# Optimization experiments

Measured on AMD Instinct MI355X. Metric: run time of the kernel, lower is better.

## Reference

```python
import jax, jax.numpy as jnp
import numpy as np

B = 4096       # batch
S = 4096       # seq_len == input_dim
DEPTH = 2
D_MODEL = 1
D_FFN = 2      # d_model * d_ffn_factor
EPS = 1e-5


def _layernorm(x, w, b):
    mu = jnp.mean(x, axis=-1, keepdims=True)
    var = jnp.mean((x - mu) ** 2, axis=-1, keepdims=True)
    return (x - mu) * jax.lax.rsqrt(var + EPS) * w + b


def setup_inputs() -> dict:
    key = jax.random.key(0)
    ks = jax.random.split(key, 16)
    sc = lambda fan_in: 1.0 / np.sqrt(fan_in)
    inp = {
        "x": jax.random.normal(ks[0], (B, S), dtype=jnp.float32),
        # per-depth stacked gMLP block params
        "ln1_w": jnp.ones((DEPTH, D_MODEL), jnp.float32),
        "ln1_b": jnp.zeros((DEPTH, D_MODEL), jnp.float32),
        "cp1_w": jax.random.uniform(ks[1], (DEPTH, D_FFN, D_MODEL), jnp.float32, -sc(D_MODEL), sc(D_MODEL)),
        "cp1_b": jax.random.uniform(ks[2], (DEPTH, D_FFN), jnp.float32, -sc(D_MODEL), sc(D_MODEL)),
        "sgu_ln_w": jnp.ones((DEPTH, D_FFN // 2), jnp.float32),
        "sgu_ln_b": jnp.zeros((DEPTH, D_FFN // 2), jnp.float32),
        "sgu_proj_w": jax.random.uniform(ks[3], (DEPTH, S, S), jnp.float32, -sc(S), sc(S)),
        "sgu_proj_b": jax.random.uniform(ks[4], (DEPTH, S), jnp.float32, -sc(S), sc(S)),
        "cp2_w": jax.random.uniform(ks[5], (DEPTH, D_MODEL, D_FFN // 2), jnp.float32, -sc(D_FFN // 2), sc(D_FFN // 2)),
        "cp2_b": jax.random.uniform(ks[6], (DEPTH, D_MODEL), jnp.float32, -sc(D_FFN // 2), sc(D_FFN // 2)),
        "pooler_w": jax.random.uniform(ks[7], (S, S), jnp.float32, -sc(S), sc(S)),
        "pooler_b": jax.random.uniform(ks[8], (S,), jnp.float32, -sc(S), sc(S)),
        "cls_w": jax.random.uniform(ks[9], (1, S), jnp.float32, -sc(S), sc(S)),
        "cls_b": jax.random.uniform(ks[10], (1,), jnp.float32, -sc(S), sc(S)),
    }
    return inp


def reference(x, ln1_w, ln1_b, cp1_w, cp1_b, sgu_ln_w, sgu_ln_b,
              sgu_proj_w, sgu_proj_b, cp2_w, cp2_b,
              pooler_w, pooler_b, cls_w, cls_b):
    gelu = lambda t: jax.nn.gelu(t, approximate=False)
    h = x[..., None]                                   # [B, S, 1]
    for i in range(DEPTH):
        res = h
        t = _layernorm(h, ln1_w[i], ln1_b[i])          # [B, S, 1]
        t = gelu(t @ cp1_w[i].T + cp1_b[i])            # [B, S, 2]
        u, v = t[..., :D_FFN // 2], t[..., D_FFN // 2:]
        v = _layernorm(v, sgu_ln_w[i], sgu_ln_b[i])
        # transpose(1,2) -> Linear(S,S) -> transpose back, fused as einsum
        v = jnp.einsum('st,btc->bsc', sgu_proj_w[i], v) + sgu_proj_b[i][:, None]
        h = u * v                                      # [B, S, 1]
        h = h @ cp2_w[i].T + cp2_b[i] + res            # [B, S, 1]
    out = h[..., 0]                                    # [B, S]
    out = gelu(out @ pooler_w.T + pooler_b)            # [B, S]
    logits = out @ cls_w.T + cls_b                     # [B, 1]
    return logits[..., 0]                              # [B]
```

## Files before the change

### kernel.cpp

```cpp
#include <hip/hip_runtime.h>


#define K_DIM 4096

typedef __bf16 bf16x8 __attribute__((ext_vector_type(8)));
typedef float f32x4 __attribute__((ext_vector_type(4)));

__device__ __forceinline__ ushort f2bf(float f) {
    unsigned int u = __float_as_uint(f);
    u = (u + 0x7fffu + ((u >> 16) & 1u)) >> 16;
    return (ushort)u;
}

__device__ __forceinline__ float gelu_exact(float x) {
    return 0.5f * x * (1.0f + erff(x * 0.70710678118654752440f));
}

__device__ __forceinline__ void gld16(const void* g, void* l) {
    __builtin_amdgcn_global_load_lds(
        (__attribute__((address_space(1))) void*)(g),
        (__attribute__((address_space(3))) void*)(l), 16, 0, 0);
}

__global__ __launch_bounds__(256) void cvt_kernel(const float* __restrict__ src,
                                                  ushort* __restrict__ dst) {
    int i = blockIdx.x * 256 + threadIdx.x;
    const float4* s4 = (const float4*)src + (size_t)i * 2;
    float4 a = s4[0], b = s4[1];
    union { ushort u[8]; uint4 v; } r;
    r.u[0] = f2bf(a.x); r.u[1] = f2bf(a.y); r.u[2] = f2bf(a.z); r.u[3] = f2bf(a.w);
    r.u[4] = f2bf(b.x); r.u[5] = f2bf(b.y); r.u[6] = f2bf(b.z); r.u[7] = f2bf(b.w);
    ((uint4*)dst)[i] = r.v;
}

__global__ __launch_bounds__(256) void rowsum_kernel(const float* __restrict__ proj_w,
                                                     const float* __restrict__ sgu_ln_b,
                                                     float* __restrict__ R) {
    int wid  = (blockIdx.x * 256 + threadIdx.x) >> 6;
    int lane = threadIdx.x & 63;
    int layer = wid >> 12;
    float beta = sgu_ln_b[layer];
    if (beta == 0.0f) {
        if (lane == 0) R[wid] = 0.0f;
        return;
    }
    const float* pr = proj_w + (size_t)wid * K_DIM;
    float s = 0.0f;
    for (int it = 0; it < 16; ++it) {
        float4 pv = *(const float4*)&pr[it * 256 + lane * 4];
        s += pv.x + pv.y + pv.z + pv.w;
    }
#pragma unroll
    for (int m = 1; m < 64; m <<= 1) s += __shfl_xor(s, m);
    if (lane == 0) R[wid] = s;
}

__global__ __launch_bounds__(256) void c_kernel(const float* __restrict__ ln1_b,
                                                const float* __restrict__ cp1_w,
                                                const float* __restrict__ cp1_b,
                                                const float* __restrict__ sgu_ln_b,
                                                const float* __restrict__ sgu_proj_b,
                                                const float* __restrict__ cp2_w,
                                                const float* __restrict__ cp2_b,
                                                const float* __restrict__ cls_b,
                                                const float* __restrict__ R,
                                                float* __restrict__ c,
                                                float* __restrict__ out) {
    int t = blockIdx.x * 256 + threadIdx.x;
    float cv = 0.0f;
#pragma unroll
    for (int i = 0; i < 2; ++i) {
        float alpha = gelu_exact(ln1_b[i] * cp1_w[i * 2 + 0] + cp1_b[i * 2 + 0]);
        float beta  = sgu_ln_b[i];
        float v     = beta * R[i * 4096 + t] + sgu_proj_b[i * 4096 + t];
        cv += alpha * v * cp2_w[i] + cp2_b[i];
    }
    c[t]   = cv;
    out[t] = cls_b[0];
}

__global__ __launch_bounds__(256) void e_kernel(const ushort* __restrict__ Pb,
                                                const float* __restrict__ c,
                                                const float* __restrict__ pooler_b,
                                                float* __restrict__ e) {
    int row  = blockIdx.x * 4 + (threadIdx.x >> 6);
    int lane = threadIdx.x & 63;
    const ushort* pr = Pb + (size_t)row * K_DIM;
    float s = 0.0f;
    for (int it = 0; it < 8; ++it) {
        int col = it * 512 + lane * 8;
        bf16x8 pv = *(const bf16x8*)&pr[col];
#pragma unroll
        for (int j = 0; j < 8; ++j) s += (float)pv[j] * c[col + j];
    }
#pragma unroll
    for (int m = 1; m < 64; m <<= 1) s += __shfl_xor(s, m);
    if (lane == 0) e[row] = s + pooler_b[row];
}

__global__ __launch_bounds__(256, 2) void gemm_kernel(const ushort* __restrict__ X,
                                                      const ushort* __restrict__ P,
                                                      const float* __restrict__ clsW,
                                                      const float* __restrict__ e,
                                                      float* __restrict__ accOut) {
    __shared__ __align__(16) ushort As[128 * 64];
    __shared__ __align__(16) ushort Bs[128 * 64];

    const int t = threadIdx.x;
    const int bCol = blockIdx.x, bRow = blockIdx.y;
    const int lane = t & 63, wv = t >> 6;
    const int g = lane >> 4, lo = lane & 15;
    const int wm = wv >> 1, wn = wv & 1;

    f32x4 zero4 = {0.f, 0.f, 0.f, 0.f};
    f32x4 acc[4][4];
#pragma unroll
    for (int mi = 0; mi < 4; ++mi)
#pragma unroll
        for (int ni = 0; ni < 4; ++ni) acc[mi][ni] = zero4;

    const int sr = t >> 3;
    const int cs = (t & 7) ^ (sr & 7);
    const ushort* gA = X + (size_t)(bRow * 128 + sr) * K_DIM + cs * 8;
    const ushort* gB = P + (size_t)(bCol * 128 + sr) * K_DIM + cs * 8;
    char* lA = (char*)As + t * 16;
    char* lB = (char*)Bs + t * 16;

    for (int k0 = 0; k0 < K_DIM; k0 += 64) {
        gld16(gA,              lA);
        gld16(gA + 32 * K_DIM, lA + 4096);
        gld16(gA + 64 * K_DIM, lA + 8192);
        gld16(gA + 96 * K_DIM, lA + 12288);
        gld16(gB,              lB);
        gld16(gB + 32 * K_DIM, lB + 4096);
        gld16(gB + 64 * K_DIM, lB + 8192);
        gld16(gB + 96 * K_DIM, lB + 12288);
        gA += 64;
        gB += 64;
        __syncthreads();

#pragma unroll
        for (int kk = 0; kk < 2; ++kk) {
            const int ch = (((kk << 2) | g) ^ (lo & 7)) * 8;
            bf16x8 af[4], bfr[4];
#pragma unroll
            for (int mi = 0; mi < 4; ++mi) {
                int row = wm * 64 + mi * 16 + lo;
                af[mi] = *(const bf16x8*)&As[row * 64 + ch];
            }
#pragma unroll
            for (int ni = 0; ni < 4; ++ni) {
                int col = wn * 64 + ni * 16 + lo;
                bfr[ni] = *(const bf16x8*)&Bs[col * 64 + ch];
            }
#pragma unroll
            for (int mi = 0; mi < 4; ++mi)
#pragma unroll
                for (int ni = 0; ni < 4; ++ni)
                    acc[mi][ni] = __builtin_amdgcn_mfma_f32_16x16x32_bf16(af[mi], bfr[ni], acc[mi][ni], 0, 0, 0);
        }
        __syncthreads();
    }

    int sColBase = bCol * 128 + wn * 64 + lo;
    float eb[4], cw[4];
#pragma unroll
    for (int ni = 0; ni < 4; ++ni) {
        int s = sColBase + ni * 16;
        eb[ni] = e[s];
        cw[ni] = clsW[s];
    }
#pragma unroll
    for (int mi = 0; mi < 4; ++mi) {
        int rowBase = bRow * 128 + wm * 64 + mi * 16 + g * 4;
#pragma unroll
        for (int r = 0; r < 4; ++r) {
            float sum = 0.0f;
#pragma unroll
            for (int ni = 0; ni < 4; ++ni) {
                float y = acc[mi][ni][r] + eb[ni];
                sum += gelu_exact(y) * cw[ni];
            }
            sum += __shfl_xor(sum, 1);
            sum += __shfl_xor(sum, 2);
            sum += __shfl_xor(sum, 4);
            sum += __shfl_xor(sum, 8);
            if (lo == 0) atomicAdd(&accOut[rowBase + r], sum);
        }
    }
}

extern "C" void kernel_launch(void* const* d_in, const int* in_sizes, int n_in,
                              void* d_out, int out_size, void* d_ws, size_t ws_size,
                              hipStream_t stream) {
    const float* x          = (const float*)d_in[0];
    const float* ln1_b      = (const float*)d_in[2];
    const float* cp1_w      = (const float*)d_in[3];
    const float* cp1_b      = (const float*)d_in[4];
    const float* sgu_ln_b   = (const float*)d_in[6];
    const float* sgu_proj_w = (const float*)d_in[7];
    const float* sgu_proj_b = (const float*)d_in[8];
    const float* cp2_w      = (const float*)d_in[9];
    const float* cp2_b      = (const float*)d_in[10];
    const float* pooler_w   = (const float*)d_in[11];
    const float* pooler_b   = (const float*)d_in[12];
    const float* cls_w      = (const float*)d_in[13];
    const float* cls_b      = (const float*)d_in[14];

    ushort* xb = (ushort*)d_ws;
    ushort* pb = xb + (size_t)K_DIM * K_DIM;
    float*  fs = (float*)(pb + (size_t)K_DIM * K_DIM);
    float* c_buf = fs;
    float* e_buf = fs + 4096;
    float* R     = fs + 8192;
    float* out   = (float*)d_out;

    cvt_kernel<<<8192, 256, 0, stream>>>(x, xb);
    cvt_kernel<<<8192, 256, 0, stream>>>(pooler_w, pb);
    rowsum_kernel<<<2048, 256, 0, stream>>>(sgu_proj_w, sgu_ln_b, R);
    c_kernel<<<16, 256, 0, stream>>>(ln1_b, cp1_w, cp1_b, sgu_ln_b, sgu_proj_b,
                                     cp2_w, cp2_b, cls_b, R, c_buf, out);
    e_kernel<<<1024, 256, 0, stream>>>(pb, c_buf, pooler_b, e_buf);
    gemm_kernel<<<dim3(32, 32), 256, 0, stream>>>(xb, pb, cls_w, e_buf, out);
}
```

Measured before the change: 412.3 us.

## Double-buffer GEMM LDS tiles with K=32 stages and merge conversion kernels

The GEMM main loop now uses two LDS buffers of half the K depth (32 instead of 64). It prefetches the next K-slice with global_load_lds while MFMAs run on the current one, and needs one barrier per iteration instead of two. The XOR swizzle is redone for the 64-byte row pitch. The two fp32-to-bf16 conversion launches are also merged into a single launch. The trade-off is twice as many loop iterations, each with less MFMA work per barrier. The prefetch is issued into the other buffer without waiting for its own completion before the barrier, so correctness depends on the barrier's implicit vmcnt wait.

```diff
diff --git a/kernel.cpp b/kernel.cpp
--- a/kernel.cpp
+++ b/kernel.cpp
@@ -22,14 +22,19 @@
         (__attribute__((address_space(3))) void*)(l), 16, 0, 0);
 }
 
-__global__ __launch_bounds__(256) void cvt_kernel(const float* __restrict__ src,
-                                                  ushort* __restrict__ dst) {
-    int i = blockIdx.x * 256 + threadIdx.x;
+__global__ __launch_bounds__(256) void cvt2_kernel(const float* __restrict__ s0,
+                                                   ushort* __restrict__ d0,
+                                                   const float* __restrict__ s1,
+                                                   ushort* __restrict__ d1) {
+    int b = blockIdx.x;
+    const float* src = (b < 8192) ? s0 : s1;
+    ushort* dst = (b < 8192) ? d0 : d1;
+    int i = (b & 8191) * 256 + threadIdx.x;
     const float4* s4 = (const float4*)src + (size_t)i * 2;
-    float4 a = s4[0], b = s4[1];
+    float4 a = s4[0], c = s4[1];
     union { ushort u[8]; uint4 v; } r;
     r.u[0] = f2bf(a.x); r.u[1] = f2bf(a.y); r.u[2] = f2bf(a.z); r.u[3] = f2bf(a.w);
-    r.u[4] = f2bf(b.x); r.u[5] = f2bf(b.y); r.u[6] = f2bf(b.z); r.u[7] = f2bf(b.w);
+    r.u[4] = f2bf(c.x); r.u[5] = f2bf(c.y); r.u[6] = f2bf(c.z); r.u[7] = f2bf(c.w);
     ((uint4*)dst)[i] = r.v;
 }
 
@@ -103,8 +108,8 @@
                                                       const float* __restrict__ clsW,
                                                       const float* __restrict__ e,
                                                       float* __restrict__ accOut) {
-    __shared__ __align__(16) ushort As[128 * 64];
-    __shared__ __align__(16) ushort Bs[128 * 64];
+    __shared__ __align__(16) ushort As[2][128 * 32];
+    __shared__ __align__(16) ushort Bs[2][128 * 32];
 
     const int t = threadIdx.x;
     const int bCol = blockIdx.x, bRow = blockIdx.y;
@@ -119,47 +124,50 @@
 #pragma unroll
         for (int ni = 0; ni < 4; ++ni) acc[mi][ni] = zero4;
 
-    const int sr = t >> 3;
-    const int cs = (t & 7) ^ (sr & 7);
-    const ushort* gA = X + (size_t)(bRow * 128 + sr) * K_DIM + cs * 8;
-    const ushort* gB = P + (size_t)(bCol * 128 + sr) * K_DIM + cs * 8;
+    const int rl = t >> 2;
+    const int cs = (t & 3) ^ ((rl >> 1) & 3);
+    const ushort* gA = X + (size_t)(bRow * 128 + rl) * K_DIM + cs * 8;
+    const ushort* gB = P + (size_t)(bCol * 128 + rl) * K_DIM + cs * 8;
     char* lA = (char*)As + t * 16;
     char* lB = (char*)Bs + t * 16;
 
-    for (int k0 = 0; k0 < K_DIM; k0 += 64) {
-        gld16(gA,              lA);
-        gld16(gA + 32 * K_DIM, lA + 4096);
-        gld16(gA + 64 * K_DIM, lA + 8192);
-        gld16(gA + 96 * K_DIM, lA + 12288);
-        gld16(gB,              lB);
-        gld16(gB + 32 * K_DIM, lB + 4096);
-        gld16(gB + 64 * K_DIM, lB + 8192);
-        gld16(gB + 96 * K_DIM, lB + 12288);
-        gA += 64;
-        gB += 64;
+    const int ch = (g ^ ((lo >> 1) & 3)) * 16;
+
+    gld16(gA,              lA);
+    gld16(gA + 64 * K_DIM, lA + 4096);
+    gld16(gB,              lB);
+    gld16(gB + 64 * K_DIM, lB + 4096);
+    __syncthreads();
+
+    int buf = 0;
+    for (int k0 = 0; k0 < K_DIM; k0 += 32) {
+        if (k0 + 32 < K_DIM) {
+            int nb = buf ^ 1;
+            gld16(gA + (k0 + 32),              lA + nb * 8192);
+            gld16(gA + (k0 + 32) + 64 * K_DIM, lA + nb * 8192 + 4096);
+            gld16(gB + (k0 + 32),              lB + nb * 8192);
+            gld16(gB + (k0 + 32) + 64 * K_DIM, lB + nb * 8192 + 4096);
+        }
+
+        bf16x8 af[4], bfr[4];
+#pragma unroll
+        for (int mi = 0; mi < 4; ++mi) {
+            int row = wm * 64 + mi * 16 + lo;
+            af[mi] = *(const bf16x8*)((const char*)As[buf] + row * 64 + ch);
+        }
+#pragma unroll
+        for (int ni = 0; ni < 4; ++ni) {
+            int col = wn * 64 + ni * 16 + lo;
+            bfr[ni] = *(const bf16x8*)((const char*)Bs[buf] + col * 64 + ch);
+        }
+#pragma unroll
+        for (int mi = 0; mi < 4; ++mi)
+#pragma unroll
+            for (int ni = 0; ni < 4; ++ni)
+                acc[mi][ni] = __builtin_amdgcn_mfma_f32_16x16x32_bf16(af[mi], bfr[ni], acc[mi][ni], 0, 0, 0);
+
         __syncthreads();
-
-#pragma unroll
-        for (int kk = 0; kk < 2; ++kk) {
-            const int ch = (((kk << 2) | g) ^ (lo & 7)) * 8;
-            bf16x8 af[4], bfr[4];
-#pragma unroll
-            for (int mi = 0; mi < 4; ++mi) {
-                int row = wm * 64 + mi * 16 + lo;
-                af[mi] = *(const bf16x8*)&As[row * 64 + ch];
-            }
-#pragma unroll
-            for (int ni = 0; ni < 4; ++ni) {
-                int col = wn * 64 + ni * 16 + lo;
-                bfr[ni] = *(const bf16x8*)&Bs[col * 64 + ch];
-            }
-#pragma unroll
-            for (int mi = 0; mi < 4; ++mi)
-#pragma unroll
-                for (int ni = 0; ni < 4; ++ni)
-                    acc[mi][ni] = __builtin_amdgcn_mfma_f32_16x16x32_bf16(af[mi], bfr[ni], acc[mi][ni], 0, 0, 0);
-        }
-        __syncthreads();
+        buf ^= 1;
     }
 
     int sColBase = bCol * 128 + wn * 64 + lo;
@@ -215,8 +223,7 @@
     float* R     = fs + 8192;
     float* out   = (float*)d_out;
 
-    cvt_kernel<<<8192, 256, 0, stream>>>(x, xb);
-    cvt_kernel<<<8192, 256, 0, stream>>>(pooler_w, pb);
+    cvt2_kernel<<<16384, 256, 0, stream>>>(x, xb, pooler_w, pb);
     rowsum_kernel<<<2048, 256, 0, stream>>>(sgu_proj_w, sgu_ln_b, R);
     c_kernel<<<16, 256, 0, stream>>>(ln1_b, cp1_w, cp1_b, sgu_ln_b, sgu_proj_b,
                                      cp2_w, cp2_b, cls_b, R, c_buf, out);
```

Measured after the change: 439.8 us. +6.7%, slower.
